# Kernel tuning notes

Measured on AMD Instinct MI355X. Metric: run time of the kernel, lower is better.

Reference implementation:

```python
import jax, jax.numpy as jnp
import numpy as np

N_NODES = 20000
IN_CH = 128
OUT_CH = 128
HEADS = 1
OB_DIM = 4
N_STEP = 32           # = HEADS*OUT_CH*8 // 32
D_PE = 16             # 32 - HEADS*16
N_EDGES = 256000


def setup_inputs() -> dict:
    key = jax.random.key(0)
    ks = jax.random.split(key, 9)
    x = jax.random.normal(ks[0], (N_NODES, IN_CH), jnp.float32)
    p_t = jax.random.normal(ks[1], (N_STEP, D_PE), jnp.float32)
    edge_index = jax.random.randint(ks[2], (2, N_EDGES), 0, N_NODES, jnp.int32)
    edge_weights = jax.random.uniform(ks[3], (N_EDGES,), jnp.float32)
    # Linear params (PyTorch default init: U(-1/sqrt(fan_in), 1/sqrt(fan_in)))
    s = 1.0 / np.sqrt(IN_CH)
    lin_value_w = jax.random.uniform(ks[4], (IN_CH, HEADS * OUT_CH), jnp.float32, -s, s)
    lin_value_b = jax.random.uniform(ks[5], (HEADS * OUT_CH,), jnp.float32, -s, s)
    inc_w = jax.random.uniform(ks[6], (IN_CH, HEADS * OUT_CH * 8), jnp.float32, -s, s)
    inc_b = jax.random.uniform(ks[7], (HEADS * OUT_CH * 8,), jnp.float32, -s, s)
    g = np.sqrt(6.0 / (N_NODES + HEADS * 16))  # glorot
    map_weights = jax.random.uniform(ks[8], (N_NODES, HEADS * 16), jnp.float32, -g, g)
    return {"x": x, "p_t": p_t, "edge_index": edge_index, "edge_weights": edge_weights,
            "lin_value_w": lin_value_w, "lin_value_b": lin_value_b,
            "inc_w": inc_w, "inc_b": inc_b, "map_weights": map_weights}


def _segment_softmax(gamma, index, num_segments):
    # PyG-style softmax over edges grouped by destination index, per column
    m = jax.ops.segment_max(gamma, index, num_segments=num_segments)     # [N, D]
    num = jnp.exp(gamma - m[index])
    den = jax.ops.segment_sum(num, index, num_segments=num_segments)    # [N, D]
    return num / den[index]


def reference(x, p_t, edge_index, edge_weights, lin_value_w, lin_value_b,
              inc_w, inc_b, map_weights):
    src = edge_index[0]   # x_j side
    dst = edge_index[1]   # x_i side (flow source_to_target)
    n_step = p_t.shape[0]
    E = src.shape[0]

    x_i = x[dst]                                             # [E, in]
    # h_W = increase_dim(x_i).view(E, n_step, 32)
    h_W = (x_i @ inc_w + inc_b).reshape(E, n_step, 32)       # [E, T, 32]
    w_v = map_weights[dst]                                   # [E, 16]
    # beta = mean(h_W * cat([w_v, p_t], -1), -1) computed without materializing aa
    beta = (jnp.einsum('etk,ek->et', h_W[:, :, :16], w_v)
            + jnp.einsum('etk,tk->et', h_W[:, :, 16:], p_t)) / 32.0   # [E, T]

    gamma = beta * edge_weights[:, None]                     # [E, T]
    gamma = jnp.repeat(gamma, OB_DIM, axis=-1)               # [E, T*ob_dim] = [E, H*out]
    all_edge_weights = jnp.mean(gamma, axis=1)               # [E]

    K = int(E * 0.5)
    _, top_idx = jax.lax.top_k(all_edge_weights, K)          # top-K edges
    gamma = gamma[top_idx]                                   # [K, H*out]
    x_i = x_i[top_idx]                                       # [K, in]
    # NOTE: the module re-points aggregation index to edge_index[0] (source)
    index = src[top_idx]                                     # [K]

    gamma = _segment_softmax(gamma, index, N_NODES)          # [K, H*out]

    v = jax.nn.relu(x_i @ lin_value_w + lin_value_b)         # [K, H*out]
    msg = (v.reshape(K, HEADS, OUT_CH)
           * gamma.reshape(K, HEADS, OUT_CH))                # [K, H, out]

    out = jax.ops.segment_sum(msg.reshape(K, HEADS * OUT_CH), index,
                              num_segments=N_NODES)          # scatter-add
    return out                                               # [N, H*out]
```

## Files before the change

kernel.cpp:

```cpp
#include <hip/hip_runtime.h>

#define NN 20000
#define IC 128
#define OC 128
#define NSTEP 32
#define NE 256000
#define KSEL 128000
#define NB 79
#define CH 32
#define ECH 8000
#define HPW 10000
#define CANDCAP 65536
#define NQCOL 704

struct SelState {
  unsigned long long prefix;
  unsigned r;
  unsigned selc;
  unsigned tiec;
  unsigned done[8];
};

typedef __attribute__((ext_vector_type(16))) float f16v;

__global__ void k_init(const float* __restrict__ p_t, const float* __restrict__ lin_w,
                       const float* __restrict__ lin_b,
                       const float* __restrict__ inc_w, const float* __restrict__ inc_b,
                       float* __restrict__ Wq,
                       double* __restrict__ Ud, double* __restrict__ ubd,
                       unsigned* __restrict__ hist, SelState* st) {
  int i = blockIdx.x * blockDim.x + threadIdx.x;
  if (i < 33 * NQCOL) {
    int k4 = i / NQCOL, col = i - k4 * NQCOL;
    float4 o;
    float* ov = (float*)&o;
    for (int jj = 0; jj < 4; ++jj) {
      int k = 4 * k4 + jj;
      float v = 0.f;
      if (col < 512) {
        int t = col >> 4, c = col & 15;
        if (k < 128) v = inc_w[k * 1024 + t * 32 + c];
        else if (k == 128) v = inc_b[t * 32 + c];
      } else if (col < 544) {
        int t = col - 512;
        if (k < 128) {
          float a = 0.f;
          for (int q = 0; q < 16; ++q) a += inc_w[k * 1024 + t * 32 + 16 + q] * p_t[t * 16 + q];
          v = a;
        } else if (k == 128) {
          float a = 0.f;
          for (int q = 0; q < 16; ++q) a += inc_b[t * 32 + 16 + q] * p_t[t * 16 + q];
          v = a;
        }
      } else if (col < 672) {
        int c = col - 544;
        if (k < 128) v = lin_w[k * OC + c];
        else if (k == 128) v = lin_b[c];
      }
      ov[jj] = v;
    }
    ((float4*)Wq)[i] = o;
    return;
  }
  i -= 33 * NQCOL;
  if (i < 17 * IC) {
    int c = i >> 7, k = i & 127;
    double a = 0.0;
    if (c < 16) {
      for (int t = 0; t < NSTEP; ++t) a += (double)inc_w[k * 1024 + t * 32 + c];
    } else {
      for (int t = 0; t < NSTEP; ++t)
        for (int q = 0; q < 16; ++q)
          a += (double)inc_w[k * 1024 + t * 32 + 16 + q] * (double)p_t[t * 16 + q];
    }
    Ud[c * IC + k] = a;
    return;
  }
  i -= 17 * IC;
  if (i < 17) {
    double a = 0.0;
    if (i < 16) {
      for (int t = 0; t < NSTEP; ++t) a += (double)inc_b[t * 32 + i];
    } else {
      for (int t = 0; t < NSTEP; ++t)
        for (int q = 0; q < 16; ++q)
          a += (double)inc_b[t * 32 + 16 + q] * (double)p_t[t * 16 + q];
    }
    ubd[i] = a;
    return;
  }
  i -= 17;
  if (i < 512) { hist[i] = 0u; return; }
  i -= 512;
  if (i == 0) {
    st->prefix = 0ull; st->r = KSEL; st->selc = 0u; st->tiec = 0u;
    for (int p = 0; p < 8; ++p) st->done[p] = 0u;
  }
}

#define FMA4(WV, BASE)                                                                        \
  acc[BASE+0] = fmaf(xf.x, WV[0],  fmaf(xf.y, WV[1],  fmaf(xf.z, WV[2],  fmaf(xf.w, WV[3],  acc[BASE+0])))); \
  acc[BASE+1] = fmaf(xf.x, WV[4],  fmaf(xf.y, WV[5],  fmaf(xf.z, WV[6],  fmaf(xf.w, WV[7],  acc[BASE+1])))); \
  acc[BASE+2] = fmaf(xf.x, WV[8],  fmaf(xf.y, WV[9],  fmaf(xf.z, WV[10], fmaf(xf.w, WV[11], acc[BASE+2])))); \
  acc[BASE+3] = fmaf(xf.x, WV[12], fmaf(xf.y, WV[13], fmaf(xf.z, WV[14], fmaf(xf.w, WV[15], acc[BASE+3]))));

__global__ __launch_bounds__(256) void k_node(
    const float* __restrict__ x, const float* __restrict__ mw,
    const float* __restrict__ Wq,
    float* __restrict__ beta, float* __restrict__ V) {
  __shared__ float4 xl[64 * 32];
  int tid = threadIdx.x;
  int g = blockIdx.x;
  int s = blockIdx.y;
  int n0 = g * 64;
  int nvalid = NN - n0; if (nvalid > 64) nvalid = 64;

  for (int i = tid; i < 64 * 32; i += 256) {
    int mm = i >> 5, k4 = i & 31;
    float4 v = make_float4(0.f, 0.f, 0.f, 0.f);
    if (mm < nvalid) v = ((const float4*)(x + (size_t)(n0 + mm) * IC))[k4];
    xl[(mm << 5) + ((k4 + mm) & 31)] = v;
  }
  int m = tid & 63;
  int j = __builtin_amdgcn_readfirstlane(threadIdx.x >> 6);
  __syncthreads();

  for (int r = 0; r < 2; ++r) {
    int u = s * 8 + j + r * 4;
    if (u < 32) {
      float mwr[16];
      {
        int mm = (m < nvalid) ? m : 0;
        const float4* mp = (const float4*)(mw + (size_t)(n0 + mm) * 16);
#pragma unroll
        for (int i = 0; i < 4; ++i) {
          float4 t4 = mp[i];
          mwr[4 * i] = t4.x; mwr[4 * i + 1] = t4.y; mwr[4 * i + 2] = t4.z; mwr[4 * i + 3] = t4.w;
        }
      }
      const f16v*   wb = (const f16v*)Wq + (u << 2);
      const float4* wp = (const float4*)Wq + (512 + u);
      float acc[16], accp;
      {
        const f16v* wkb = wb + 32 * 176;
        f16v b0 = wkb[0], b1 = wkb[1], b2 = wkb[2], b3 = wkb[3];
#pragma unroll
        for (int c = 0; c < 4; ++c) {
          acc[c] = b0[4 * c]; acc[4 + c] = b1[4 * c];
          acc[8 + c] = b2[4 * c]; acc[12 + c] = b3[4 * c];
        }
        accp = wp[32 * NQCOL].x;
      }
      f16v w0 = wb[0], w1 = wb[1], w2 = wb[2], w3 = wb[3];
      float4 pw = wp[0];
      for (int k4 = 0; k4 < 32; ++k4) {
        f16v nw0, nw1, nw2, nw3; float4 npw;
        if (k4 < 31) {
          const f16v* wn = wb + (k4 + 1) * 176;
          nw0 = wn[0]; nw1 = wn[1]; nw2 = wn[2]; nw3 = wn[3];
          npw = wp[(k4 + 1) * NQCOL];
        }
        float4 xf = xl[(m << 5) + ((k4 + m) & 31)];
        FMA4(w0, 0) FMA4(w1, 4) FMA4(w2, 8) FMA4(w3, 12)
        accp = fmaf(xf.x, pw.x, fmaf(xf.y, pw.y, fmaf(xf.z, pw.z, fmaf(xf.w, pw.w, accp))));
        if (k4 < 31) { w0 = nw0; w1 = nw1; w2 = nw2; w3 = nw3; pw = npw; }
      }
      float bs = accp;
#pragma unroll
      for (int c = 0; c < 16; ++c) bs = fmaf(acc[c], mwr[c], bs);
      if (m < nvalid) beta[(size_t)(n0 + m) * NSTEP + u] = bs * (1.f / 32.f);
    } else {
      int vg = u - 32;
      int vc0 = vg << 4;
      const f16v* wb = (const f16v*)Wq + 136 + (vg << 2);
      float acc[16];
      {
        const f16v* wkb = wb + 32 * 176;
        f16v b0 = wkb[0], b1 = wkb[1], b2 = wkb[2], b3 = wkb[3];
#pragma unroll
        for (int c = 0; c < 4; ++c) {
          acc[c] = b0[4 * c]; acc[4 + c] = b1[4 * c];
          acc[8 + c] = b2[4 * c]; acc[12 + c] = b3[4 * c];
        }
      }
      f16v w0 = wb[0], w1 = wb[1], w2 = wb[2], w3 = wb[3];
      for (int k4 = 0; k4 < 32; ++k4) {
        f16v nw0, nw1, nw2, nw3;
        if (k4 < 31) {
          const f16v* wn = wb + (k4 + 1) * 176;
          nw0 = wn[0]; nw1 = wn[1]; nw2 = wn[2]; nw3 = wn[3];
        }
        float4 xf = xl[(m << 5) + ((k4 + m) & 31)];
        FMA4(w0, 0) FMA4(w1, 4) FMA4(w2, 8) FMA4(w3, 12)
        if (k4 < 31) { w0 = nw0; w1 = nw1; w2 = nw2; w3 = nw3; }
      }
      if (m < nvalid) {
        float* vout = V + (size_t)(n0 + m) * OC + vc0;
#pragma unroll
        for (int q = 0; q < 4; ++q) {
          float4 o;
          o.x = fmaxf(acc[4 * q], 0.f);     o.y = fmaxf(acc[4 * q + 1], 0.f);
          o.z = fmaxf(acc[4 * q + 2], 0.f); o.w = fmaxf(acc[4 * q + 3], 0.f);
          ((float4*)vout)[q] = o;
        }
      }
    }
  }
}

__global__ __launch_bounds__(256) void k_s64(
    const float* __restrict__ x, const float* __restrict__ mw,
    const double* __restrict__ Ud, const double* __restrict__ ubd,
    double* __restrict__ s64) {
  int tid = blockIdx.x * 256 + threadIdx.x;
  int m = tid >> 4, c = tid & 15;
  if (m >= NN) return;
  const float*  xr  = x + (size_t)m * IC;
  const double* uc  = Ud + c * IC;
  const double* u16 = Ud + 16 * IC;
  double a = 0.0, a16 = 0.0;
  for (int k = 0; k < IC; k += 4) {
    float4 xv = *(const float4*)(xr + k);
    a   = fma((double)xv.x, uc[k],      a);
    a   = fma((double)xv.y, uc[k + 1],  a);
    a   = fma((double)xv.z, uc[k + 2],  a);
    a   = fma((double)xv.w, uc[k + 3],  a);
    a16 = fma((double)xv.x, u16[k],     a16);
    a16 = fma((double)xv.y, u16[k + 1], a16);
    a16 = fma((double)xv.z, u16[k + 2], a16);
    a16 = fma((double)xv.w, u16[k + 3], a16);
  }
  double part = (a + ubd[c]) * (double)mw[m * 16 + c];
#pragma unroll
  for (int d = 1; d < 16; d <<= 1) part += __shfl_xor(part, d, 64);
  if (c == 0) s64[m] = (part + a16 + ubd[16]) * (1.0 / 1024.0);
}

__global__ void k_keysel(const int* __restrict__ ei, const float* __restrict__ ew,
                         const double* __restrict__ s64,
                         unsigned long long* __restrict__ keys,
                         unsigned* __restrict__ hist, SelState* st) {
  __shared__ unsigned h[256], suf[256];
  __shared__ int last;
  int tid = threadIdx.x;
  h[tid] = 0u;
  if (tid == 0) last = 0;
  __syncthreads();
  for (int e = blockIdx.x * 256 + tid; e < NE; e += gridDim.x * 256) {
    int d = ei[NE + e];
    double v = s64[d] * (double)ew[e];
    unsigned long long u = (unsigned long long)__double_as_longlong(v);
    u = (u & 0x8000000000000000ull) ? ~u : (u | 0x8000000000000000ull);
    keys[e] = u;
    atomicAdd(&h[(unsigned)(u >> 56)], 1u);
  }
  __syncthreads();
  if (h[tid]) atomicAdd(&hist[tid], h[tid]);
  __threadfence();
  __syncthreads();
  if (tid == 0) {
    if (atomicAdd(&st->done[0], 1u) == gridDim.x - 1) last = 1;
  }
  __syncthreads();
  if (!last) return;
  unsigned c = atomicAdd(&hist[tid], 0u);
  suf[tid] = c;
  __syncthreads();
  for (int d = 1; d < 256; d <<= 1) {
    unsigned v = (tid + d < 256) ? suf[tid + d] : 0u;
    __syncthreads();
    suf[tid] += v;
    __syncthreads();
  }
  unsigned r = st->r;
  unsigned exc = suf[tid] - c;
  if (exc < r && exc + c >= r) {
    st->prefix = (unsigned long long)tid;
    st->r = r - exc;
  }
}

__global__ void k_radix1(const unsigned long long* __restrict__ keys,
                         unsigned* __restrict__ hist, SelState* st) {
  __shared__ unsigned h[256], suf[256];
  __shared__ int last;
  int tid = threadIdx.x;
  h[tid] = 0u;
  if (tid == 0) last = 0;
  unsigned long long pref = st->prefix;
  __syncthreads();
  unsigned* hp = hist + 256;
  for (int e = blockIdx.x * 256 + tid; e < NE; e += gridDim.x * 256) {
    unsigned long long k = keys[e];
    if ((k >> 56) == pref)
      atomicAdd(&h[(unsigned)((k >> 48) & 255ull)], 1u);
  }
  __syncthreads();
  if (h[tid]) atomicAdd(&hp[tid], h[tid]);
  __threadfence();
  __syncthreads();
  if (tid == 0) {
    if (atomicAdd(&st->done[1], 1u) == gridDim.x - 1) last = 1;
  }
  __syncthreads();
  if (!last) return;
  unsigned c = atomicAdd(&hp[tid], 0u);
  suf[tid] = c;
  __syncthreads();
  for (int d = 1; d < 256; d <<= 1) {
    unsigned v = (tid + d < 256) ? suf[tid + d] : 0u;
    __syncthreads();
    suf[tid] += v;
    __syncthreads();
  }
  unsigned r = st->r;
  unsigned exc = suf[tid] - c;
  if (exc < r && exc + c >= r) {
    st->prefix = (st->prefix << 8) | (unsigned long long)tid;
    st->r = r - exc;
  }
}

__global__ void k_candsel(const unsigned long long* __restrict__ keys,
                          SelState* st,
                          unsigned long long* __restrict__ flags,
                          unsigned long long* __restrict__ candk, int* __restrict__ cande) {
  __shared__ unsigned h[256], suf[256];
  __shared__ unsigned long long spref;
  __shared__ unsigned sr;
  __shared__ int last;
  int tid = threadIdx.x;
  if (tid == 0) last = 0;
  unsigned P16 = (unsigned)st->prefix;
  for (int e = blockIdx.x * 256 + tid; e < NE; e += gridDim.x * 256) {
    unsigned long long k = keys[e];
    unsigned t16 = (unsigned)(k >> 48);
    unsigned long long bal = __ballot(t16 > P16);
    if ((tid & 63) == 0) flags[e >> 6] = bal;
    if (t16 == P16) {
      unsigned pos = atomicAdd(&st->tiec, 1u);
      if (pos < CANDCAP) { candk[pos] = k; cande[pos] = e; }
    }
  }
  __threadfence();
  __syncthreads();
  if (tid == 0) {
    if (atomicAdd(&st->done[2], 1u) == gridDim.x - 1) last = 1;
  }
  __syncthreads();
  if (!last) return;
  unsigned C = atomicAdd(&st->tiec, 0u); if (C > CANDCAP) C = CANDCAP;
  if (tid == 0) { spref = (unsigned long long)P16; sr = st->r; }
  __syncthreads();
  for (int p = 2; p < 8; ++p) {
    h[tid] = 0u;
    __syncthreads();
    int shift = 56 - 8 * p;
    unsigned long long pf = spref;
    unsigned r = sr;
    for (unsigned i = tid; i < C; i += 256) {
      unsigned long long k = candk[i];
      if ((k >> (shift + 8)) == pf) atomicAdd(&h[(unsigned)((k >> shift) & 255ull)], 1u);
    }
    __syncthreads();
    suf[tid] = h[tid];
    __syncthreads();
    for (int d = 1; d < 256; d <<= 1) {
      unsigned v = (tid + d < 256) ? suf[tid + d] : 0u;
      __syncthreads();
      suf[tid] += v;
      __syncthreads();
    }
    unsigned exc = suf[tid] - h[tid];
    if (exc < r && exc + h[tid] >= r) {
      spref = (pf << 8) | (unsigned long long)tid;
      sr = r - exc;
    }
    __syncthreads();
  }
  unsigned long long T = spref;
  unsigned needed = sr;
  for (unsigned i = tid; i < C; i += 256) {
    unsigned long long k = candk[i];
    int e2 = cande[i];
    bool take = false;
    if (k > T) take = true;
    else if (k == T) {
      unsigned rank = 0;
      for (unsigned q = 0; q < C; ++q)
        rank += (candk[q] == T && cande[q] < e2) ? 1u : 0u;
      take = (rank < needed);
    }
    if (take) atomicOr(&flags[e2 >> 6], 1ull << (e2 & 63));
  }
}

__global__ __launch_bounds__(256) void k_count1(const int* __restrict__ ei,
                                                const unsigned long long* __restrict__ flags,
                                                unsigned* __restrict__ hpart) {
  __shared__ unsigned hp[HPW];
  int tid = threadIdx.x;
  for (int i = tid; i < HPW; i += 256) hp[i] = 0u;
  __syncthreads();
  int base = blockIdx.x * ECH;
  int lim = base + ECH; if (lim > NE) lim = NE;
  for (int k0 = 0; k0 < 32; k0 += 4) {
    int nn[4]; bool tk[4];
#pragma unroll
    for (int q = 0; q < 4; ++q) {
      int e = base + tid + (k0 + q) * 256;
      bool valid = e < lim;
      unsigned long long w = valid ? flags[e >> 6] : 0ull;
      nn[q] = valid ? ei[e] : 0;
      tk[q] = valid && ((w >> (e & 63)) & 1ull);
    }
#pragma unroll
    for (int q = 0; q < 4; ++q)
      if (tk[q]) atomicAdd(&hp[nn[q] >> 1], 1u << ((nn[q] & 1) * 16));
  }
  __syncthreads();
  unsigned* dst = hpart + (size_t)blockIdx.x * HPW;
  for (int i = tid; i < HPW; i += 256) dst[i] = hp[i];
}

__global__ void k_prefA(const unsigned* __restrict__ hpart,
                        unsigned short* __restrict__ hoffl,
                        unsigned* __restrict__ cnt, unsigned* __restrict__ bsum,
                        unsigned* __restrict__ bbase, unsigned* __restrict__ offar,
                        SelState* st) {
  __shared__ unsigned sd[256];
  __shared__ int last;
  int tid = threadIdx.x;
  if (tid == 0) last = 0;
  int n = blockIdx.x * 256 + tid;
  unsigned tot = 0u;
  if (n < NN) {
    int half = (n & 1) * 16;
    int wi = n >> 1;
#pragma unroll 4
    for (int b = 0; b < CH; ++b) {
      hoffl[(size_t)b * NN + n] = (unsigned short)tot;
      tot += (hpart[(size_t)b * HPW + wi] >> half) & 0xFFFFu;
    }
    cnt[n] = tot;
  }
  sd[tid] = (n < NN) ? tot : 0u;
  __syncthreads();
  for (int s = 128; s > 0; s >>= 1) {
    if (tid < s) sd[tid] += sd[tid + s];
    __syncthreads();
  }
  if (tid == 0) bsum[blockIdx.x] = sd[0];
  __threadfence();
  __syncthreads();
  if (tid == 0) {
    if (atomicAdd(&st->done[3], 1u) == gridDim.x - 1) last = 1;
  }
  __syncthreads();
  if (!last) return;
  unsigned v = (tid < NB) ? bsum[tid] : 0u;
  sd[tid] = v;
  __syncthreads();
  for (int d = 1; d < 256; d <<= 1) {
    unsigned u = (tid >= d) ? sd[tid - d] : 0u;
    __syncthreads();
    sd[tid] += u;
    __syncthreads();
  }
  if (tid < NB) bbase[tid] = sd[tid] - v;
  if (tid == NB - 1) offar[NN] = sd[tid];
}

__global__ void k_prefB(const unsigned* __restrict__ cnt, const unsigned* __restrict__ bbase,
                        const unsigned short* __restrict__ hoffl,
                        unsigned* __restrict__ offar, unsigned* __restrict__ hoffabs) {
  __shared__ unsigned sd[256];
  int tid = threadIdx.x;
  int n = blockIdx.x * 256 + tid;
  unsigned v = (n < NN) ? cnt[n] : 0u;
  sd[tid] = v;
  __syncthreads();
  for (int d = 1; d < 256; d <<= 1) {
    unsigned u = (tid >= d) ? sd[tid - d] : 0u;
    __syncthreads();
    sd[tid] += u;
    __syncthreads();
  }
  if (n < NN) {
    unsigned off = bbase[blockIdx.x] + sd[tid] - v;
    offar[n] = off;
#pragma unroll 4
    for (int b = 0; b < CH; ++b)
      hoffabs[(size_t)b * NN + n] = off + (unsigned)hoffl[(size_t)b * NN + n];
  }
}

__global__ __launch_bounds__(256) void k_scatterC(const int* __restrict__ ei,
                                                  const unsigned long long* __restrict__ flags,
                                                  const unsigned* __restrict__ hoffabs,
                                                  int* __restrict__ csr) {
  __shared__ unsigned rel[HPW];
  int tid = threadIdx.x;
  for (int i = tid; i < HPW; i += 256) rel[i] = 0u;
  __syncthreads();
  int base = blockIdx.x * ECH;
  int lim = base + ECH; if (lim > NE) lim = NE;
  const unsigned* hb = hoffabs + (size_t)blockIdx.x * NN;
  for (int k0 = 0; k0 < 32; k0 += 4) {
    int nn[4]; bool tk[4]; unsigned hb4[4];
#pragma unroll
    for (int q = 0; q < 4; ++q) {
      int e = base + tid + (k0 + q) * 256;
      bool valid = e < lim;
      unsigned long long w = valid ? flags[e >> 6] : 0ull;
      tk[q] = valid && ((w >> (e & 63)) & 1ull);
      nn[q] = valid ? ei[e] : 0;
      hb4[q] = tk[q] ? hb[nn[q]] : 0u;
    }
#pragma unroll
    for (int q = 0; q < 4; ++q) {
      if (tk[q]) {
        int half = (nn[q] & 1) * 16;
        unsigned old = atomicAdd(&rel[nn[q] >> 1], 1u << half);
        unsigned r = (old >> half) & 0xFFFFu;
        unsigned pos = hb4[q] + r;
        if (pos < KSEL) csr[pos] = base + tid + (k0 + q) * 256;
      }
    }
  }
}

__global__ __launch_bounds__(128) void k_out(
    const int* __restrict__ ei, const float* __restrict__ ew,
    const float* __restrict__ beta, const float* __restrict__ V,
    const unsigned* __restrict__ offar, const int* __restrict__ csr,
    float* __restrict__ out) {
  __shared__ float B[32][NSTEP];
  __shared__ float m[NSTEP], den[NSTEP], scale[NSTEP];
  __shared__ int dl[32];
  __shared__ float ewl[32];
  int n = blockIdx.x, tid = threadIdx.x;
  unsigned beg = offar[n], end = offar[n + 1];
  if (end > (unsigned)KSEL) end = KSEL;
  if (beg > end) beg = end;
  if (tid < NSTEP) { m[tid] = -INFINITY; den[tid] = 0.f; }
  float acc = 0.f;
  int c = tid, tq = tid >> 2;
  __syncthreads();

  for (unsigned cb = beg; cb < end; cb += 32u) {
    unsigned ce = end - cb; if (ce > 32u) ce = 32u;
    if (tid < (int)ce) {
      int e = csr[cb + tid];
      dl[tid] = ei[NE + e];
      ewl[tid] = ew[e];
    }
    __syncthreads();
    for (int idx = tid; idx < (int)ce * NSTEP; idx += 128) {
      int el = idx >> 5, t = idx & 31;
      B[el][t] = beta[(size_t)dl[el] * NSTEP + t] * ewl[el];
    }
    __syncthreads();
    if (tid < NSTEP) {
      int t = tid;
      float mc = -INFINITY;
      for (int el = 0; el < (int)ce; ++el) mc = fmaxf(mc, B[el][t]);
      float mnew = fmaxf(m[t], mc);
      float sc = expf(m[t] - mnew);
      float s = 0.f;
      for (int el = 0; el < (int)ce; ++el) {
        float g = expf(B[el][t] - mnew);
        B[el][t] = g;
        s += g;
      }
      den[t] = den[t] * sc + s;
      m[t] = mnew;
      scale[t] = sc;
    }
    __syncthreads();
    acc *= scale[tq];
    for (int el = 0; el < (int)ce; ++el)
      acc += V[(size_t)dl[el] * OC + c] * B[el][tq];
    __syncthreads();
  }
  float d = den[tq];
  out[(size_t)n * OC + c] = (d > 0.f) ? acc / d : 0.f;
}

extern "C" void kernel_launch(void* const* d_in, const int* in_sizes, int n_in,
                              void* d_out, int out_size, void* d_ws, size_t ws_size,
                              hipStream_t stream) {
  const float* x     = (const float*)d_in[0];
  const float* p_t   = (const float*)d_in[1];
  const int*   ei    = (const int*)d_in[2];
  const float* ew    = (const float*)d_in[3];
  const float* lin_w = (const float*)d_in[4];
  const float* lin_b = (const float*)d_in[5];
  const float* inc_w = (const float*)d_in[6];
  const float* inc_b = (const float*)d_in[7];
  const float* mw    = (const float*)d_in[8];
  float* out = (float*)d_out;

  char* w = (char*)d_ws;
  size_t off = 0;
  auto alloc = [&](size_t b) -> void* {
    void* p = w + off;
    off += (b + 511) & ~(size_t)511;
    return p;
  };
  float*  Wq    = (float*)alloc((size_t)33 * NQCOL * 4 * 4);
  double* Ud    = (double*)alloc((size_t)17 * IC * 8);
  double* ubd   = (double*)alloc(17 * 8);
  float*  beta  = (float*)alloc((size_t)NN * NSTEP * 4);
  double* s64   = (double*)alloc((size_t)NN * 8);
  float*  V     = (float*)alloc((size_t)NN * OC * 4);
  unsigned long long* keys  = (unsigned long long*)alloc((size_t)NE * 8);
  unsigned long long* flags = (unsigned long long*)alloc((size_t)(NE / 64) * 8);
  unsigned long long* candk = (unsigned long long*)alloc((size_t)CANDCAP * 8);
  int*      cande  = (int*)alloc((size_t)CANDCAP * 4);
  unsigned* hpart  = (unsigned*)alloc((size_t)CH * HPW * 4);
  unsigned short* hoffl = (unsigned short*)alloc((size_t)CH * NN * 2);
  unsigned* hoffabs = (unsigned*)alloc((size_t)CH * NN * 4);
  unsigned* cnt    = (unsigned*)alloc((size_t)NN * 4);
  unsigned* offar  = (unsigned*)alloc((size_t)(NN + 1) * 4);
  int*      csr    = (int*)alloc((size_t)KSEL * 4);
  unsigned* hist   = (unsigned*)alloc(512 * 4);
  unsigned* bsum   = (unsigned*)alloc(NB * 4);
  unsigned* bbase  = (unsigned*)alloc(NB * 4);
  SelState* st     = (SelState*)alloc(sizeof(SelState));
  if (off > ws_size) return;

  int init_threads = 33 * NQCOL + 17 * IC + 17 + 512 + 1;
  k_init<<<(init_threads + 255) / 256, 256, 0, stream>>>(p_t, lin_w, lin_b, inc_w, inc_b,
                                                         Wq, Ud, ubd, hist, st);
  k_node<<<dim3((NN + 63) / 64, 5), 256, 0, stream>>>(x, mw, Wq, beta, V);
  k_s64<<<(NN * 16 + 255) / 256, 256, 0, stream>>>(x, mw, Ud, ubd, s64);
  k_keysel<<<256, 256, 0, stream>>>(ei, ew, s64, keys, hist, st);
  k_radix1<<<256, 256, 0, stream>>>(keys, hist, st);
  k_candsel<<<256, 256, 0, stream>>>(keys, st, flags, candk, cande);
  k_count1<<<CH, 256, 0, stream>>>(ei, flags, hpart);
  k_prefA<<<NB, 256, 0, stream>>>(hpart, hoffl, cnt, bsum, bbase, offar, st);
  k_prefB<<<NB, 256, 0, stream>>>(cnt, bbase, hoffl, offar, hoffabs);
  k_scatterC<<<CH, 256, 0, stream>>>(ei, flags, hoffabs, csr);
  k_out<<<NN, 128, 0, stream>>>(ei, ew, beta, V, offar, csr, out);
}
```

Before: 335.7 us.

## Fuse s64 scoring into node kernel, double CSR chunk count, drop hoffabs buffer

Folds the k_s64 double-precision score computation into k_node as an extra grid slice that reuses the shared-memory x tile, removing one launch and a second read of x. It also splits edges into 64 chunks of 4000 for the count and scatter kernels to raise parallelism. The per-chunk absolute offset array is no longer materialized in k_prefB; k_scatterC instead computes offar plus the local offset on the fly. The risk is that the extra s==5 slice is a serial double-precision loop per thread, and that k_prefA's handling of CH must stay consistent with 64 chunks.

```diff
diff --git a/kernel.cpp b/kernel.cpp
--- a/kernel.cpp
+++ b/kernel.cpp
@@ -7,8 +7,9 @@
 #define NE 256000
 #define KSEL 128000
 #define NB 79
-#define CH 32
-#define ECH 8000
+#define CH 64
+#define ECH 4000
+#define RND 16
 #define HPW 10000
 #define CANDCAP 65536
 #define NQCOL 704
@@ -106,8 +107,9 @@
 
 __global__ __launch_bounds__(256) void k_node(
     const float* __restrict__ x, const float* __restrict__ mw,
-    const float* __restrict__ Wq,
-    float* __restrict__ beta, float* __restrict__ V) {
+    const float* __restrict__ Wq, const double* __restrict__ Ud,
+    const double* __restrict__ ubd,
+    float* __restrict__ beta, float* __restrict__ V, double* __restrict__ s64) {
   __shared__ float4 xl[64 * 32];
   int tid = threadIdx.x;
   int g = blockIdx.x;
@@ -124,6 +126,40 @@
   int m = tid & 63;
   int j = __builtin_amdgcn_readfirstlane(threadIdx.x >> 6);
   __syncthreads();
+
+  if (s == 5) {
+    int m2 = tid >> 2, sub = tid & 3;
+    int mm = (m2 < nvalid) ? m2 : 0;
+    double part = 0.0;
+    for (int cc = 0; cc < 4; ++cc) {
+      int c = sub * 4 + cc;
+      const double* uc = Ud + c * IC;
+      double a = 0.0;
+      for (int k4 = 0; k4 < 32; ++k4) {
+        float4 xv = xl[(m2 << 5) + ((k4 + m2) & 31)];
+        a = fma((double)xv.x, uc[4 * k4],     a);
+        a = fma((double)xv.y, uc[4 * k4 + 1], a);
+        a = fma((double)xv.z, uc[4 * k4 + 2], a);
+        a = fma((double)xv.w, uc[4 * k4 + 3], a);
+      }
+      part += (a + ubd[c]) * (double)mw[(size_t)(n0 + mm) * 16 + c];
+    }
+    const double* u16p = Ud + 16 * IC;
+    double a16 = 0.0;
+    for (int k4 = sub * 8; k4 < sub * 8 + 8; ++k4) {
+      float4 xv = xl[(m2 << 5) + ((k4 + m2) & 31)];
+      a16 = fma((double)xv.x, u16p[4 * k4],     a16);
+      a16 = fma((double)xv.y, u16p[4 * k4 + 1], a16);
+      a16 = fma((double)xv.z, u16p[4 * k4 + 2], a16);
+      a16 = fma((double)xv.w, u16p[4 * k4 + 3], a16);
+    }
+    double tot = part + a16;
+    tot += __shfl_xor(tot, 1, 64);
+    tot += __shfl_xor(tot, 2, 64);
+    if (sub == 0 && m2 < nvalid)
+      s64[n0 + m2] = (tot + ubd[16]) * (1.0 / 1024.0);
+    return;
+  }
 
   for (int r = 0; r < 2; ++r) {
     int u = s * 8 + j + r * 4;
@@ -208,34 +244,6 @@
   }
 }
 
-__global__ __launch_bounds__(256) void k_s64(
-    const float* __restrict__ x, const float* __restrict__ mw,
-    const double* __restrict__ Ud, const double* __restrict__ ubd,
-    double* __restrict__ s64) {
-  int tid = blockIdx.x * 256 + threadIdx.x;
-  int m = tid >> 4, c = tid & 15;
-  if (m >= NN) return;
-  const float*  xr  = x + (size_t)m * IC;
-  const double* uc  = Ud + c * IC;
-  const double* u16 = Ud + 16 * IC;
-  double a = 0.0, a16 = 0.0;
-  for (int k = 0; k < IC; k += 4) {
-    float4 xv = *(const float4*)(xr + k);
-    a   = fma((double)xv.x, uc[k],      a);
-    a   = fma((double)xv.y, uc[k + 1],  a);
-    a   = fma((double)xv.z, uc[k + 2],  a);
-    a   = fma((double)xv.w, uc[k + 3],  a);
-    a16 = fma((double)xv.x, u16[k],     a16);
-    a16 = fma((double)xv.y, u16[k + 1], a16);
-    a16 = fma((double)xv.z, u16[k + 2], a16);
-    a16 = fma((double)xv.w, u16[k + 3], a16);
-  }
-  double part = (a + ubd[c]) * (double)mw[m * 16 + c];
-#pragma unroll
-  for (int d = 1; d < 16; d <<= 1) part += __shfl_xor(part, d, 64);
-  if (c == 0) s64[m] = (part + a16 + ubd[16]) * (1.0 / 1024.0);
-}
-
 __global__ void k_keysel(const int* __restrict__ ei, const float* __restrict__ ew,
                          const double* __restrict__ s64,
                          unsigned long long* __restrict__ keys,
@@ -404,7 +412,7 @@
   __syncthreads();
   int base = blockIdx.x * ECH;
   int lim = base + ECH; if (lim > NE) lim = NE;
-  for (int k0 = 0; k0 < 32; k0 += 4) {
+  for (int k0 = 0; k0 < RND; k0 += 4) {
     int nn[4]; bool tk[4];
 #pragma unroll
     for (int q = 0; q < 4; ++q) {
@@ -472,8 +480,7 @@
 }
 
 __global__ void k_prefB(const unsigned* __restrict__ cnt, const unsigned* __restrict__ bbase,
-                        const unsigned short* __restrict__ hoffl,
-                        unsigned* __restrict__ offar, unsigned* __restrict__ hoffabs) {
+                        unsigned* __restrict__ offar) {
   __shared__ unsigned sd[256];
   int tid = threadIdx.x;
   int n = blockIdx.x * 256 + tid;
@@ -486,18 +493,13 @@
     sd[tid] += u;
     __syncthreads();
   }
-  if (n < NN) {
-    unsigned off = bbase[blockIdx.x] + sd[tid] - v;
-    offar[n] = off;
-#pragma unroll 4
-    for (int b = 0; b < CH; ++b)
-      hoffabs[(size_t)b * NN + n] = off + (unsigned)hoffl[(size_t)b * NN + n];
-  }
+  if (n < NN) offar[n] = bbase[blockIdx.x] + sd[tid] - v;
 }
 
 __global__ __launch_bounds__(256) void k_scatterC(const int* __restrict__ ei,
                                                   const unsigned long long* __restrict__ flags,
-                                                  const unsigned* __restrict__ hoffabs,
+                                                  const unsigned* __restrict__ offar,
+                                                  const unsigned short* __restrict__ hoffl,
                                                   int* __restrict__ csr) {
   __shared__ unsigned rel[HPW];
   int tid = threadIdx.x;
@@ -505,8 +507,8 @@
   __syncthreads();
   int base = blockIdx.x * ECH;
   int lim = base + ECH; if (lim > NE) lim = NE;
-  const unsigned* hb = hoffabs + (size_t)blockIdx.x * NN;
-  for (int k0 = 0; k0 < 32; k0 += 4) {
+  const unsigned short* hl = hoffl + (size_t)blockIdx.x * NN;
+  for (int k0 = 0; k0 < RND; k0 += 4) {
     int nn[4]; bool tk[4]; unsigned hb4[4];
 #pragma unroll
     for (int q = 0; q < 4; ++q) {
@@ -515,7 +517,7 @@
       unsigned long long w = valid ? flags[e >> 6] : 0ull;
       tk[q] = valid && ((w >> (e & 63)) & 1ull);
       nn[q] = valid ? ei[e] : 0;
-      hb4[q] = tk[q] ? hb[nn[q]] : 0u;
+      hb4[q] = tk[q] ? (offar[nn[q]] + (unsigned)hl[nn[q]]) : 0u;
     }
 #pragma unroll
     for (int q = 0; q < 4; ++q) {
@@ -620,7 +622,6 @@
   int*      cande  = (int*)alloc((size_t)CANDCAP * 4);
   unsigned* hpart  = (unsigned*)alloc((size_t)CH * HPW * 4);
   unsigned short* hoffl = (unsigned short*)alloc((size_t)CH * NN * 2);
-  unsigned* hoffabs = (unsigned*)alloc((size_t)CH * NN * 4);
   unsigned* cnt    = (unsigned*)alloc((size_t)NN * 4);
   unsigned* offar  = (unsigned*)alloc((size_t)(NN + 1) * 4);
   int*      csr    = (int*)alloc((size_t)KSEL * 4);
@@ -633,14 +634,13 @@
   int init_threads = 33 * NQCOL + 17 * IC + 17 + 512 + 1;
   k_init<<<(init_threads + 255) / 256, 256, 0, stream>>>(p_t, lin_w, lin_b, inc_w, inc_b,
                                                          Wq, Ud, ubd, hist, st);
-  k_node<<<dim3((NN + 63) / 64, 5), 256, 0, stream>>>(x, mw, Wq, beta, V);
-  k_s64<<<(NN * 16 + 255) / 256, 256, 0, stream>>>(x, mw, Ud, ubd, s64);
+  k_node<<<dim3((NN + 63) / 64, 6), 256, 0, stream>>>(x, mw, Wq, Ud, ubd, beta, V, s64);
   k_keysel<<<256, 256, 0, stream>>>(ei, ew, s64, keys, hist, st);
   k_radix1<<<256, 256, 0, stream>>>(keys, hist, st);
   k_candsel<<<256, 256, 0, stream>>>(keys, st, flags, candk, cande);
   k_count1<<<CH, 256, 0, stream>>>(ei, flags, hpart);
   k_prefA<<<NB, 256, 0, stream>>>(hpart, hoffl, cnt, bsum, bbase, offar, st);
-  k_prefB<<<NB, 256, 0, stream>>>(cnt, bbase, hoffl, offar, hoffabs);
-  k_scatterC<<<CH, 256, 0, stream>>>(ei, flags, hoffabs, csr);
+  k_prefB<<<NB, 256, 0, stream>>>(cnt, bbase, offar);
+  k_scatterC<<<CH, 256, 0, stream>>>(ei, flags, offar, hoffl, csr);
   k_out<<<NN, 128, 0, stream>>>(ei, ew, beta, V, offar, csr, out);
 }
```

Result: slower. 446.1 us (+32.9%).
